# Performance work log

Hardware: AMD Instinct MI355X
Metric: run time of the kernel (lower is better)

The kernel has to match this reference:

```python
import jax, jax.numpy as jnp
import jax.lax as lax
import numpy as np
import math

B, T_FRAMES, H, W = 32, 8, 14, 14
C, CA = 768, 384
L = H * W + 1


def setup_inputs() -> dict:
    key = jax.random.key(0)
    ks = jax.random.split(key, 7)
    s = 0.02
    return {
        "x": jax.random.normal(ks[0], (B * T_FRAMES, L, C), dtype=jnp.float32),
        "W1": jax.random.normal(ks[1], (CA, C), dtype=jnp.float32) * s,
        "b1": jnp.zeros((CA,), dtype=jnp.float32),
        "conv_w": jax.random.normal(ks[2], (CA, 1, 3, 3, 3), dtype=jnp.float32) * s,
        "conv_b": jnp.zeros((CA,), dtype=jnp.float32),
        "W2": jax.random.normal(ks[3], (C, CA), dtype=jnp.float32) * s,
        "b2": jnp.zeros((C,), dtype=jnp.float32),
        "T": T_FRAMES,
    }


def reference(x, W1, b1, conv_w, conv_b, W2, b2, T):
    BT, Lx, Cx = x.shape
    Bb = BT // T
    Ca = W1.shape[0]
    Hh = Ww = int(round(math.sqrt(Lx - 1)))
    # fc1 on all tokens except CLS: [BT, L-1, Ca]
    h = jnp.einsum("blc,ac->bla", x[:, 1:, :], W1) + b1
    # -> [B, Ca, T, H, W] for depthwise 3d conv (groups = Ca)
    h = h.reshape(Bb, T, Hh, Ww, Ca).transpose(0, 4, 1, 2, 3)
    h = lax.conv_general_dilated(
        h, conv_w,
        window_strides=(1, 1, 1),
        padding=[(1, 1), (1, 1), (1, 1)],
        dimension_numbers=("NCDHW", "OIDHW", "NCDHW"),
        feature_group_count=Ca,
    ) + conv_b[None, :, None, None, None]
    # back to [BT, L-1, Ca]
    h = h.transpose(0, 2, 3, 4, 1).reshape(BT, Lx - 1, Ca)
    # fc2: [BT, L-1, C]
    h = jnp.einsum("bla,ca->blc", h, W2) + b2
    # residual add onto non-CLS tokens
    return x.at[:, 1:, :].add(h)
```

## Files before the change

kernel.cpp:

```cpp
#include <hip/hip_runtime.h>
#include <stdint.h>

#define BTOT   256
#define LX     197
#define CDIM   768
#define CADIM  384
#define TFR    8
#define LM1    196
#define MTOT   50176

typedef unsigned short u16;
typedef short          bf16x8 __attribute__((ext_vector_type(8)));
typedef unsigned short u16x4  __attribute__((ext_vector_type(4)));
typedef unsigned short u16x8  __attribute__((ext_vector_type(8)));
typedef float          f32x4  __attribute__((ext_vector_type(4)));

typedef const __attribute__((address_space(1))) void gvoid_t;
typedef __attribute__((address_space(3))) void       svoid_t;

static __device__ __forceinline__ u16 f2bf(float f) {
  union { float f; uint32_t u; } v; v.f = f;
  uint32_t u = v.u;
  return (u16)((u + 0x7FFFu + ((u >> 16) & 1u)) >> 16);
}
static __device__ __forceinline__ float bf2f(u16 h) {
  union { uint32_t u; float f; } v; v.u = ((uint32_t)h) << 16;
  return v.f;
}

__global__ void prep_small(const float4* __restrict__ x4, float4* __restrict__ out4,
                           const float* __restrict__ W1, const float* __restrict__ W2,
                           const float* __restrict__ cw, u16* __restrict__ w1b,
                           u16* __restrict__ w2b, float* __restrict__ cwT) {
  int i = blockIdx.x * blockDim.x + threadIdx.x;
  if (i < CADIM * CDIM) { w1b[i] = f2bf(W1[i]); w2b[i] = f2bf(W2[i]); }
  if (i < CADIM * 27) {
    int a = i / 27; int tap = i - a * 27;
    cwT[tap * CADIM + a] = cw[i];
  }
  if (i < BTOT * 192) {
    int f = i / 192, v = i - f * 192;
    size_t off = (size_t)f * (LX * CDIM / 4) + v;
    out4[off] = x4[off];
  }
}


#define GEMM_STAGE2(bufidx, k0)                                            \
  {                                                                        \
    _Pragma("unroll")                                                      \
    for (int s = 0; s < 2; ++s) {                                          \
      __builtin_amdgcn_global_load_lds((gvoid_t*)(A + aoff[s] + (k0)),     \
          (svoid_t*)(As + (bufidx) * 4096 + ldst[s]), 16, 0, 0);           \
      __builtin_amdgcn_global_load_lds((gvoid_t*)(Bw + boff[s] + (k0)),    \
          (svoid_t*)(Bs + (bufidx) * 4096 + ldst[s]), 16, 0, 0);           \
    }                                                                      \
  }

#define GEMM_STAGE_B(bufidx, k0)                                           \
  {                                                                        \
    _Pragma("unroll")                                                      \
    for (int s = 0; s < 2; ++s) {                                          \
      __builtin_amdgcn_global_load_lds((gvoid_t*)(Bw + boff[s] + (k0)),    \
          (svoid_t*)(Bs + (bufidx) * 4096 + ldst[s]), 16, 0, 0);           \
    }                                                                      \
  }

#define GEMM_COMPUTE(bufidx)                                               \
  {                                                                        \
    const u16* Ab = As + (bufidx) * 4096;                                  \
    const u16* Bb = Bs + (bufidx) * 4096;                                  \
    bf16x8 af[4], bfr[4];                                                  \
    _Pragma("unroll")                                                      \
    for (int i = 0; i < 4; i++) af[i] = *(const bf16x8*)&Ab[abase + i * 512]; \
    _Pragma("unroll")                                                      \
    for (int j = 0; j < 4; j++) bfr[j] = *(const bf16x8*)&Bb[bbase + j * 512]; \
    _Pragma("unroll")                                                      \
    for (int i = 0; i < 4; i++)                                            \
      _Pragma("unroll")                                                    \
      for (int j = 0; j < 4; j++)                                          \
        acc[i][j] = __builtin_amdgcn_mfma_f32_16x16x32_bf16(af[i], bfr[j], acc[i][j], 0, 0, 0); \
  }

#define WRITE_A(bufidx)                                                    \
  {                                                                        \
    _Pragma("unroll")                                                      \
    for (int s = 0; s < 4; ++s) {                                          \
      u16x4 o;                                                             \
      o[0] = f2bf(areg[s].x); o[1] = f2bf(areg[s].y);                      \
      o[2] = f2bf(areg[s].z); o[3] = f2bf(areg[s].w);                      \
      *(u16x4*)&As[(bufidx) * 4096 + awst[s]] = o;                         \
    }                                                                      \
  }

__global__ __launch_bounds__(256) void fc1_gemm(
    const float* __restrict__ X,
    const u16* __restrict__ Bw,
    const float* __restrict__ bias,
    u16* __restrict__ Hout)
{
  __shared__ __align__(16) u16 As[2 * 128 * 32];
  __shared__ __align__(16) u16 Bs[2 * 128 * 32];
  const int tid  = threadIdx.x;
  const int lane = tid & 63;
  const int wave = tid >> 6;
  const int m0 = blockIdx.x * 128;
  const int n0 = blockIdx.y * 128;
  const int lm = lane & 15;
  const int lk = lane >> 4;
  const int wm = (wave & 1) * 64;
  const int wn = (wave >> 1) * 64;

  const int u   = (lane & 7) ^ (lane >> 3);
  const int rr  = 2 * (lane >> 3) + (u >> 2);
  const int cko = (u & 3) * 8;
  size_t boff[2];
  int ldst[2];
#pragma unroll
  for (int s = 0; s < 2; ++s) {
    int row = wave * 32 + s * 16 + rr;
    boff[s] = (size_t)(n0 + row) * CDIM + cko;
    ldst[s] = (wave * 16 + s * 8) * 64;
  }

  const int g = tid >> 3;
  const int q = tid & 7;
  size_t arow[4];
  int awst[4];
#pragma unroll
  for (int s = 0; s < 4; ++s) {
    int row = g + 32 * s;
    int tok = m0 + row;
    int bt = tok / LM1;
    int l  = tok - bt * LM1;
    arow[s] = (size_t)(bt * LX + 1 + l) * CDIM + q * 4;
    int R    = row >> 1;
    int uu   = (row & 1) * 4 + (q >> 1);
    int slot = uu ^ (R & 7);
    awst[s]  = R * 64 + slot * 8 + (q & 1) * 4;
  }

  const int lmh   = lm >> 1;
  const int slotp = (((lm & 1) << 2) | lk) ^ lmh;
  const int abase = ((wm >> 1) + lmh) * 64 + slotp * 8;
  const int bbase = ((wn >> 1) + lmh) * 64 + slotp * 8;

  f32x4 acc[4][4];
#pragma unroll
  for (int i = 0; i < 4; i++)
#pragma unroll
    for (int j = 0; j < 4; j++) acc[i][j] = (f32x4)0.0f;

  float4 areg[4];
#pragma unroll
  for (int s = 0; s < 4; ++s) areg[s] = *(const float4*)(X + arow[s]);
  GEMM_STAGE_B(0, 0);
  WRITE_A(0);
  __syncthreads();

  int cur = 0;
  for (int kt = 0; kt < 23; ++kt) {
    const int k1 = (kt + 1) * 32;
#pragma unroll
    for (int s = 0; s < 4; ++s) areg[s] = *(const float4*)(X + arow[s] + k1);
    GEMM_STAGE_B(cur ^ 1, k1);
    GEMM_COMPUTE(cur);
    WRITE_A(cur ^ 1);
    __syncthreads();
    cur ^= 1;
  }
  GEMM_COMPUTE(cur);

#pragma unroll
  for (int i = 0; i < 4; i++) {
    int rbase = m0 + wm + i * 16 + lk * 4;
#pragma unroll
    for (int j = 0; j < 4; j++) {
      int col = n0 + wn + j * 16 + lm;
      float bv = bias[col];
#pragma unroll
      for (int r = 0; r < 4; r++)
        Hout[(rbase + r) * CADIM + col] = f2bf(acc[i][j][r] + bv);
    }
  }
}

__global__ __launch_bounds__(256) void dwconv(
    const u16* __restrict__ h1, const float* __restrict__ cwT,
    const float* __restrict__ cb, u16* __restrict__ h2)
{
  int idx = blockIdx.x * blockDim.x + threadIdx.x;
  int cg = idx % 48;
  int rest = idx / 48;
  int wp = rest % 7; rest /= 7;
  int hp = rest % 7; rest /= 7;
  int t = rest & 7;
  int frame = rest;
  int a0 = cg * 8;
  int h0 = hp * 2, w0 = wp * 2;

  float acc[2][2][8];
#pragma unroll
  for (int c = 0; c < 8; ++c) {
    float bv = cb[a0 + c];
    acc[0][0][c] = bv; acc[0][1][c] = bv; acc[1][0][c] = bv; acc[1][1][c] = bv;
  }

#pragma unroll
  for (int dt = -1; dt <= 1; ++dt) {
    int tt = t + dt;
    if (tt < 0 || tt >= TFR) continue;
    float wreg[9][8];
#pragma unroll
    for (int j = 0; j < 9; ++j) {
      const float* wp8 = cwT + ((dt + 1) * 9 + j) * CADIM + a0;
#pragma unroll
      for (int c = 0; c < 8; ++c) wreg[j][c] = wp8[c];
    }
    const u16* fbase = h1 + (size_t)(frame + dt) * LM1 * CADIM + a0;
#pragma unroll
    for (int ih = 0; ih < 4; ++ih) {
      int hh = h0 - 1 + ih;
      if (hh < 0 || hh >= 14) continue;
#pragma unroll
      for (int iw = 0; iw < 4; ++iw) {
        int ww = w0 - 1 + iw;
        if (ww < 0 || ww >= 14) continue;
        bf16x8 v = *(const bf16x8*)(fbase + (hh * 14 + ww) * CADIM);
        float vf[8];
#pragma unroll
        for (int c = 0; c < 8; ++c) vf[c] = bf2f((u16)v[c]);
#pragma unroll
        for (int oh = 0; oh < 2; ++oh) {
          if (ih - 1 - oh < -1 || ih - 1 - oh > 1) continue;
#pragma unroll
          for (int ow = 0; ow < 2; ++ow) {
            if (iw - 1 - ow < -1 || iw - 1 - ow > 1) continue;
            int j = (ih - oh) * 3 + (iw - ow);
#pragma unroll
            for (int c = 0; c < 8; ++c)
              acc[oh][ow][c] += vf[c] * wreg[j][c];
          }
        }
      }
    }
  }
  const size_t obase = (size_t)frame * LM1 * CADIM + a0;
#pragma unroll
  for (int oh = 0; oh < 2; ++oh)
#pragma unroll
    for (int ow = 0; ow < 2; ++ow) {
      u16x8 o;
#pragma unroll
      for (int c = 0; c < 8; ++c) o[c] = f2bf(acc[oh][ow][c]);
      *(u16x8*)(h2 + obase + ((size_t)(h0 + oh) * 14 + w0 + ow) * CADIM) = o;
    }
}

__global__ __launch_bounds__(256) void fc2_gemm(
    const u16* __restrict__ A,
    const u16* __restrict__ Bw,
    const float* __restrict__ bias,
    const float* __restrict__ x,
    float* __restrict__ out)
{
  __shared__ __align__(16) u16 As[2 * 128 * 32];
  __shared__ __align__(16) u16 Bs[2 * 128 * 32];
  const int tid  = threadIdx.x;
  const int lane = tid & 63;
  const int wave = tid >> 6;
  const int m0 = blockIdx.x * 128;
  const int n0 = blockIdx.y * 128;
  const int lm = lane & 15;
  const int lk = lane >> 4;
  const int wm = (wave & 1) * 64;
  const int wn = (wave >> 1) * 64;

  const int u   = (lane & 7) ^ (lane >> 3);
  const int rr  = 2 * (lane >> 3) + (u >> 2);
  const int cko = (u & 3) * 8;
  size_t aoff[2], boff[2];
  int ldst[2];
#pragma unroll
  for (int s = 0; s < 2; ++s) {
    int row = wave * 32 + s * 16 + rr;
    aoff[s] = (size_t)(m0 + row) * CADIM + cko;
    boff[s] = (size_t)(n0 + row) * CADIM + cko;
    ldst[s] = (wave * 16 + s * 8) * 64;
  }

  const int lmh   = lm >> 1;
  const int slotp = (((lm & 1) << 2) | lk) ^ lmh;
  const int abase = ((wm >> 1) + lmh) * 64 + slotp * 8;
  const int bbase = ((wn >> 1) + lmh) * 64 + slotp * 8;

  f32x4 acc[4][4];
#pragma unroll
  for (int i = 0; i < 4; i++)
#pragma unroll
    for (int j = 0; j < 4; j++) acc[i][j] = (f32x4)0.0f;

  GEMM_STAGE2(0, 0);
  __syncthreads();
  int cur = 0;
  for (int kt = 0; kt < 11; ++kt) {
    GEMM_STAGE2(cur ^ 1, (kt + 1) * 32);
    GEMM_COMPUTE(cur);
    __syncthreads();
    cur ^= 1;
  }
  GEMM_COMPUTE(cur);

  float bv[4];
#pragma unroll
  for (int j = 0; j < 4; j++) bv[j] = bias[n0 + wn + j * 16 + lm];
#pragma unroll
  for (int i = 0; i < 4; i++) {
    int rbase = m0 + wm + i * 16 + lk * 4;
    size_t orow[4];
#pragma unroll
    for (int r = 0; r < 4; r++) {
      int tok = rbase + r;
      int bt = tok / LM1;
      int l  = tok - bt * LM1;
      orow[r] = (size_t)(bt * LX + 1 + l) * CDIM + (n0 + wn + lm);
    }
    float xv[4][4];
#pragma unroll
    for (int r = 0; r < 4; r++)
#pragma unroll
      for (int j = 0; j < 4; j++)
        xv[r][j] = x[orow[r] + j * 16];
#pragma unroll
    for (int r = 0; r < 4; r++)
#pragma unroll
      for (int j = 0; j < 4; j++)
        out[orow[r] + j * 16] = xv[r][j] + acc[i][j][r] + bv[j];
  }
}

extern "C" void kernel_launch(void* const* d_in, const int* in_sizes, int n_in,
                              void* d_out, int out_size, void* d_ws, size_t ws_size,
                              hipStream_t stream) {
  const float* x  = (const float*)d_in[0];
  const float* W1 = (const float*)d_in[1];
  const float* b1 = (const float*)d_in[2];
  const float* cw = (const float*)d_in[3];
  const float* cb = (const float*)d_in[4];
  const float* W2 = (const float*)d_in[5];
  const float* b2 = (const float*)d_in[6];
  float* out = (float*)d_out;

  char* ws = (char*)d_ws;
  u16*   w1b = (u16*)(ws + 0);
  u16*   w2b = (u16*)(ws + 589824);
  float* cwT = (float*)(ws + 1179648);
  u16*   h1  = (u16*)(ws + 1245184);
  u16*   h2  = (u16*)(ws + 39780352);

  prep_small<<<1152, 256, 0, stream>>>((const float4*)x, (float4*)out,
                                       W1, W2, cw, w1b, w2b, cwT);
  fc1_gemm<<<dim3(MTOT / 128, CADIM / 128), 256, 0, stream>>>(x, w1b, b1, h1);
  dwconv  <<<(BTOT * 49 * 48) / 256, 256, 0, stream>>>(h1, cwT, cb, h2);
  fc2_gemm<<<dim3(MTOT / 128, CDIM / 128), 256, 0, stream>>>(h2, w2b, b2, x, out);
}
```

Baseline: 458.4 us.

## Deepen fc1 A-operand prefetch with register double-buffering and manual waitcnt barriers

```diff
diff --git a/kernel.cpp b/kernel.cpp
--- a/kernel.cpp
+++ b/kernel.cpp
@@ -1,4 +1,5 @@
 #include <hip/hip_runtime.h>
+#include <hip/hip_bf16.h>
 #include <stdint.h>
 
 #define BTOT   256
@@ -26,6 +27,11 @@
 static __device__ __forceinline__ float bf2f(u16 h) {
   union { uint32_t u; float f; } v; v.u = ((uint32_t)h) << 16;
   return v.f;
+}
+static __device__ __forceinline__ u16 f2bf_hw(float f) {
+  union { __hip_bfloat16 b; u16 u; } v;
+  v.b = __float2bfloat16(f);
+  return v.u;
 }
 
 __global__ void prep_small(const float4* __restrict__ x4, float4* __restrict__ out4,
@@ -82,15 +88,28 @@
         acc[i][j] = __builtin_amdgcn_mfma_f32_16x16x32_bf16(af[i], bfr[j], acc[i][j], 0, 0, 0); \
   }
 
-#define WRITE_A(bufidx)                                                    \
+#define WRITE_A_REG(bufidx, R)                                             \
   {                                                                        \
     _Pragma("unroll")                                                      \
     for (int s = 0; s < 4; ++s) {                                          \
       u16x4 o;                                                             \
-      o[0] = f2bf(areg[s].x); o[1] = f2bf(areg[s].y);                      \
-      o[2] = f2bf(areg[s].z); o[3] = f2bf(areg[s].w);                      \
+      o[0] = f2bf_hw(R[s].x); o[1] = f2bf_hw(R[s].y);                      \
+      o[2] = f2bf_hw(R[s].z); o[3] = f2bf_hw(R[s].w);                      \
       *(u16x4*)&As[(bufidx) * 4096 + awst[s]] = o;                         \
     }                                                                      \
+  }
+
+#define FC1_STEP(T, P, CUR, NXT)                                           \
+  {                                                                        \
+    GEMM_STAGE_B((P) ^ 1, ((T) + 1) * 32);                                 \
+    __builtin_amdgcn_sched_barrier(0);         \
+    WRITE_A_REG((P) ^ 1, CUR);                                             \
+    _Pragma("unroll")                                                      \
+    for (int s = 0; s < 4; ++s)                                            \
+      NXT[s] = *(const float4*)(X + arow[s] + ((T) + 2) * 32);             \
+    GEMM_COMPUTE(P);                                                       \
+    asm volatile("s_waitcnt vmcnt(4) lgkmcnt(0)" ::: "memory");            \
+    __builtin_amdgcn_s_barrier();                                          \
   }
 
 __global__ __launch_bounds__(256) void fc1_gemm(
@@ -151,25 +170,28 @@
 #pragma unroll
     for (int j = 0; j < 4; j++) acc[i][j] = (f32x4)0.0f;
 
-  float4 areg[4];
-#pragma unroll
-  for (int s = 0; s < 4; ++s) areg[s] = *(const float4*)(X + arow[s]);
+  float4 aregA[4], aregB[4];
+
+#pragma unroll
+  for (int s = 0; s < 4; ++s) aregA[s] = *(const float4*)(X + arow[s]);
   GEMM_STAGE_B(0, 0);
-  WRITE_A(0);
-  __syncthreads();
-
-  int cur = 0;
-  for (int kt = 0; kt < 23; ++kt) {
-    const int k1 = (kt + 1) * 32;
-#pragma unroll
-    for (int s = 0; s < 4; ++s) areg[s] = *(const float4*)(X + arow[s] + k1);
-    GEMM_STAGE_B(cur ^ 1, k1);
-    GEMM_COMPUTE(cur);
-    WRITE_A(cur ^ 1);
-    __syncthreads();
-    cur ^= 1;
-  }
-  GEMM_COMPUTE(cur);
+  __builtin_amdgcn_sched_barrier(0);
+  WRITE_A_REG(0, aregA);
+#pragma unroll
+  for (int s = 0; s < 4; ++s) aregA[s] = *(const float4*)(X + arow[s] + 32);
+  asm volatile("s_waitcnt vmcnt(4) lgkmcnt(0)" ::: "memory");
+  __builtin_amdgcn_s_barrier();
+
+  for (int t = 0; t < 22; t += 2) {
+    FC1_STEP(t,     0, aregA, aregB);
+    FC1_STEP(t + 1, 1, aregB, aregA);
+  }
+  GEMM_STAGE_B(1, 23 * 32);
+  WRITE_A_REG(1, aregA);
+  GEMM_COMPUTE(0);
+  asm volatile("s_waitcnt vmcnt(0) lgkmcnt(0)" ::: "memory");
+  __builtin_amdgcn_s_barrier();
+  GEMM_COMPUTE(1);
 
 #pragma unroll
   for (int i = 0; i < 4; i++) {
```

After: 479.7 us. 1.05x slower.

## Widen fc1 tile to full N=384 so X is read and converted once

Applied to the files above, without the earlier changes.

```diff
diff --git a/kernel.cpp b/kernel.cpp
--- a/kernel.cpp
+++ b/kernel.cpp
@@ -1,4 +1,5 @@
 #include <hip/hip_runtime.h>
+#include <hip/hip_bf16.h>
 #include <stdint.h>
 
 #define BTOT   256
@@ -26,6 +27,11 @@
 static __device__ __forceinline__ float bf2f(u16 h) {
   union { uint32_t u; float f; } v; v.u = ((uint32_t)h) << 16;
   return v.f;
+}
+static __device__ __forceinline__ u16 f2bf_hw(float f) {
+  union { __hip_bfloat16 b; u16 u; } v;
+  v.b = __float2bfloat16(f);
+  return v.u;
 }
 
 __global__ void prep_small(const float4* __restrict__ x4, float4* __restrict__ out4,
@@ -52,15 +58,6 @@
     for (int s = 0; s < 2; ++s) {                                          \
       __builtin_amdgcn_global_load_lds((gvoid_t*)(A + aoff[s] + (k0)),     \
           (svoid_t*)(As + (bufidx) * 4096 + ldst[s]), 16, 0, 0);           \
-      __builtin_amdgcn_global_load_lds((gvoid_t*)(Bw + boff[s] + (k0)),    \
-          (svoid_t*)(Bs + (bufidx) * 4096 + ldst[s]), 16, 0, 0);           \
-    }                                                                      \
-  }
-
-#define GEMM_STAGE_B(bufidx, k0)                                           \
-  {                                                                        \
-    _Pragma("unroll")                                                      \
-    for (int s = 0; s < 2; ++s) {                                          \
       __builtin_amdgcn_global_load_lds((gvoid_t*)(Bw + boff[s] + (k0)),    \
           (svoid_t*)(Bs + (bufidx) * 4096 + ldst[s]), 16, 0, 0);           \
     }                                                                      \
@@ -82,62 +79,58 @@
         acc[i][j] = __builtin_amdgcn_mfma_f32_16x16x32_bf16(af[i], bfr[j], acc[i][j], 0, 0, 0); \
   }
 
-#define WRITE_A(bufidx)                                                    \
-  {                                                                        \
-    _Pragma("unroll")                                                      \
-    for (int s = 0; s < 4; ++s) {                                          \
-      u16x4 o;                                                             \
-      o[0] = f2bf(areg[s].x); o[1] = f2bf(areg[s].y);                      \
-      o[2] = f2bf(areg[s].z); o[3] = f2bf(areg[s].w);                      \
-      *(u16x4*)&As[(bufidx) * 4096 + awst[s]] = o;                         \
-    }                                                                      \
-  }
-
-__global__ __launch_bounds__(256) void fc1_gemm(
+__global__ __launch_bounds__(768, 2) void fc1_gemm(
     const float* __restrict__ X,
     const u16* __restrict__ Bw,
     const float* __restrict__ bias,
     u16* __restrict__ Hout)
 {
   __shared__ __align__(16) u16 As[2 * 128 * 32];
-  __shared__ __align__(16) u16 Bs[2 * 128 * 32];
+  __shared__ __align__(16) u16 Bs[2 * 384 * 32];
   const int tid  = threadIdx.x;
   const int lane = tid & 63;
   const int wave = tid >> 6;
   const int m0 = blockIdx.x * 128;
-  const int n0 = blockIdx.y * 128;
   const int lm = lane & 15;
   const int lk = lane >> 4;
-  const int wm = (wave & 1) * 64;
-  const int wn = (wave >> 1) * 64;
-
-  const int u   = (lane & 7) ^ (lane >> 3);
-  const int rr  = 2 * (lane >> 3) + (u >> 2);
-  const int cko = (u & 3) * 8;
-  size_t boff[2];
-  int ldst[2];
-#pragma unroll
-  for (int s = 0; s < 2; ++s) {
-    int row = wave * 32 + s * 16 + rr;
-    boff[s] = (size_t)(n0 + row) * CDIM + cko;
-    ldst[s] = (wave * 16 + s * 8) * 64;
-  }
+  const int wr = wave / 6;
+  const int wc = wave - wr * 6;
+  const int wm = wr * 64;
+  const int wn = wc * 64;
+  const bool is_a = (wave < 4);
 
   const int g = tid >> 3;
   const int q = tid & 7;
   size_t arow[4];
   int awst[4];
-#pragma unroll
-  for (int s = 0; s < 4; ++s) {
-    int row = g + 32 * s;
-    int tok = m0 + row;
-    int bt = tok / LM1;
-    int l  = tok - bt * LM1;
-    arow[s] = (size_t)(bt * LX + 1 + l) * CDIM + q * 4;
-    int R    = row >> 1;
-    int uu   = (row & 1) * 4 + (q >> 1);
-    int slot = uu ^ (R & 7);
-    awst[s]  = R * 64 + slot * 8 + (q & 1) * 4;
+  if (is_a) {
+#pragma unroll
+    for (int s = 0; s < 4; ++s) {
+      int row = g + 32 * s;
+      int tok = m0 + row;
+      int bt = tok / LM1;
+      int l  = tok - bt * LM1;
+      arow[s] = (size_t)(bt * LX + 1 + l) * CDIM + q * 4;
+      int R    = row >> 1;
+      int uu   = (row & 1) * 4 + (q >> 1);
+      int slot = uu ^ (R & 7);
+      awst[s]  = R * 64 + slot * 8 + (q & 1) * 4;
+    }
+  }
+
+  const int wb  = wave - 4;
+  const int u   = (lane & 7) ^ (lane >> 3);
+  const int rr  = 2 * (lane >> 3) + (u >> 2);
+  const int cko = (u & 3) * 8;
+  size_t boff[3];
+  int ldst[3];
+  if (!is_a) {
+#pragma unroll
+    for (int s = 0; s < 3; ++s) {
+      int row = wb * 48 + s * 16 + rr;
+      boff[s] = (size_t)row * CDIM + cko;
+      ldst[s] = (wb * 24 + s * 8) * 64;
+    }
   }
 
   const int lmh   = lm >> 1;
@@ -152,31 +145,85 @@
     for (int j = 0; j < 4; j++) acc[i][j] = (f32x4)0.0f;
 
   float4 areg[4];
-#pragma unroll
-  for (int s = 0; s < 4; ++s) areg[s] = *(const float4*)(X + arow[s]);
-  GEMM_STAGE_B(0, 0);
-  WRITE_A(0);
+
+  if (is_a) {
+#pragma unroll
+    for (int s = 0; s < 4; ++s) areg[s] = *(const float4*)(X + arow[s]);
+#pragma unroll
+    for (int s = 0; s < 4; ++s) {
+      u16x4 o;
+      o[0] = f2bf_hw(areg[s].x); o[1] = f2bf_hw(areg[s].y);
+      o[2] = f2bf_hw(areg[s].z); o[3] = f2bf_hw(areg[s].w);
+      *(u16x4*)&As[awst[s]] = o;
+    }
+  } else {
+#pragma unroll
+    for (int s = 0; s < 3; ++s)
+      __builtin_amdgcn_global_load_lds((gvoid_t*)(Bw + boff[s]),
+          (svoid_t*)(Bs + ldst[s]), 16, 0, 0);
+  }
   __syncthreads();
 
   int cur = 0;
   for (int kt = 0; kt < 23; ++kt) {
     const int k1 = (kt + 1) * 32;
-#pragma unroll
-    for (int s = 0; s < 4; ++s) areg[s] = *(const float4*)(X + arow[s] + k1);
-    GEMM_STAGE_B(cur ^ 1, k1);
-    GEMM_COMPUTE(cur);
-    WRITE_A(cur ^ 1);
+    const int nb = cur ^ 1;
+    if (is_a) {
+#pragma unroll
+      for (int s = 0; s < 4; ++s) areg[s] = *(const float4*)(X + arow[s] + k1);
+    } else {
+#pragma unroll
+      for (int s = 0; s < 3; ++s)
+        __builtin_amdgcn_global_load_lds((gvoid_t*)(Bw + boff[s] + k1),
+            (svoid_t*)(Bs + nb * 12288 + ldst[s]), 16, 0, 0);
+    }
+    {
+      const u16* Ab = As + cur * 4096;
+      const u16* Bb = Bs + cur * 12288;
+      bf16x8 af[4], bfr[4];
+#pragma unroll
+      for (int i = 0; i < 4; i++) af[i] = *(const bf16x8*)&Ab[abase + i * 512];
+#pragma unroll
+      for (int j = 0; j < 4; j++) bfr[j] = *(const bf16x8*)&Bb[bbase + j * 512];
+#pragma unroll
+      for (int i = 0; i < 4; i++)
+#pragma unroll
+        for (int j = 0; j < 4; j++)
+          acc[i][j] = __builtin_amdgcn_mfma_f32_16x16x32_bf16(af[i], bfr[j], acc[i][j], 0, 0, 0);
+    }
+    if (is_a) {
+#pragma unroll
+      for (int s = 0; s < 4; ++s) {
+        u16x4 o;
+        o[0] = f2bf_hw(areg[s].x); o[1] = f2bf_hw(areg[s].y);
+        o[2] = f2bf_hw(areg[s].z); o[3] = f2bf_hw(areg[s].w);
+        *(u16x4*)&As[nb * 4096 + awst[s]] = o;
+      }
+    }
     __syncthreads();
     cur ^= 1;
   }
-  GEMM_COMPUTE(cur);
+  {
+    const u16* Ab = As + cur * 4096;
+    const u16* Bb = Bs + cur * 12288;
+    bf16x8 af[4], bfr[4];
+#pragma unroll
+    for (int i = 0; i < 4; i++) af[i] = *(const bf16x8*)&Ab[abase + i * 512];
+#pragma unroll
+    for (int j = 0; j < 4; j++) bfr[j] = *(const bf16x8*)&Bb[bbase + j * 512];
+#pragma unroll
+    for (int i = 0; i < 4; i++)
+#pragma unroll
+      for (int j = 0; j < 4; j++)
+        acc[i][j] = __builtin_amdgcn_mfma_f32_16x16x32_bf16(af[i], bfr[j], acc[i][j], 0, 0, 0);
+  }
 
 #pragma unroll
   for (int i = 0; i < 4; i++) {
     int rbase = m0 + wm + i * 16 + lk * 4;
 #pragma unroll
     for (int j = 0; j < 4; j++) {
-      int col = n0 + wn + j * 16 + lm;
+      int col = wn + j * 16 + lm;
       float bv = bias[col];
 #pragma unroll
       for (int r = 0; r < 4; r++)
@@ -360,7 +407,7 @@
 
   prep_small<<<1152, 256, 0, stream>>>((const float4*)x, (float4*)out,
                                        W1, W2, cw, w1b, w2b, cwT);
-  fc1_gemm<<<dim3(MTOT / 128, CADIM / 128), 256, 0, stream>>>(x, w1b, b1, h1);
+  fc1_gemm<<<MTOT / 128, 768, 0, stream>>>(x, w1b, b1, h1);
   dwconv  <<<(BTOT * 49 * 48) / 256, 256, 0, stream>>>(h1, cwT, cb, h2);
   fc2_gemm<<<dim3(MTOT / 128, CDIM / 128), 256, 0, stream>>>(h2, w2b, b2, x, out);
 }
```

After: 446.0 us. 1.03x faster.
